# Kernel optimization log

Hardware: AMD Instinct MI355X
Metric: run time of the kernel (lower is better)

## Reference

```python
import jax, jax.numpy as jnp
import numpy as np

N, E, FD, H, NG, LAT = 20000, 320000, 64, 4, 64, 512


def _gat(x, W, a_src, a_dst, b, src, dst):
    # x: [N, in]; W: [H*FD, in]; a_src/a_dst: [H, FD]; b: [H*FD]
    h = (x @ W.T).reshape(N, H, FD)
    s = jnp.sum(h * a_src, -1)   # [N, H]
    d = jnp.sum(h * a_dst, -1)   # [N, H]
    e = jax.nn.leaky_relu(s[src] + d[dst], negative_slope=0.2)  # [E', H]
    m = jax.ops.segment_max(e, dst, num_segments=N)
    ex = jnp.exp(e - m[dst])
    den = jax.ops.segment_sum(ex, dst, num_segments=N)
    alpha = ex / den[dst]                                        # [E', H]
    out = jax.ops.segment_sum(alpha[:, :, None] * h[src], dst, num_segments=N)
    return out.reshape(N, H * FD) + b


def setup_inputs() -> dict:
    key = jax.random.key(0)
    ks = jax.random.split(key, 24)
    inp = {}
    inp['street_feature'] = jax.random.normal(ks[0], (N, 128), jnp.float32)
    inp['building_feature'] = jax.random.normal(ks[1], (N, 5), jnp.float32)
    sm = jax.random.randint(ks[2], (N, 1), 0, 2).astype(jnp.float32)
    inp['street_mask'] = sm
    inp['building_mask'] = 1.0 - sm
    inp['edge_index'] = jax.random.randint(ks[3], (2, E), 0, N, dtype=jnp.int32)
    # batch: sorted graph ids covering all NG graphs (no empty segments)
    rest = jax.random.randint(ks[4], (N - NG,), 0, NG, dtype=jnp.int32)
    inp['batch'] = jnp.sort(jnp.concatenate([jnp.arange(NG, dtype=jnp.int32), rest]))

    def lin(k, o, i):
        s = 1.0 / np.sqrt(i)
        return jax.random.uniform(k, (o, i), jnp.float32, -s, s)

    inp['street_W'] = lin(ks[5], FD, 128); inp['street_b'] = jnp.zeros((FD,), jnp.float32)
    inp['building_W'] = lin(ks[6], FD, 5); inp['building_b'] = jnp.zeros((FD,), jnp.float32)
    inp['W1'] = lin(ks[7], H * FD, FD)
    inp['a_src1'] = jax.random.normal(ks[8], (H, FD), jnp.float32) * 0.1
    inp['a_dst1'] = jax.random.normal(ks[9], (H, FD), jnp.float32) * 0.1
    inp['b1'] = jnp.zeros((H * FD,), jnp.float32)
    inp['W2'] = lin(ks[10], H * FD, H * FD)
    inp['a_src2'] = jax.random.normal(ks[11], (H, FD), jnp.float32) * 0.1
    inp['a_dst2'] = jax.random.normal(ks[12], (H, FD), jnp.float32) * 0.1
    inp['b2'] = jnp.zeros((H * FD,), jnp.float32)
    inp['W3'] = lin(ks[13], H * FD, H * FD)
    inp['a_src3'] = jax.random.normal(ks[14], (H, FD), jnp.float32) * 0.1
    inp['a_dst3'] = jax.random.normal(ks[15], (H, FD), jnp.float32) * 0.1
    inp['b3'] = jnp.zeros((H * FD,), jnp.float32)
    agg_in = FD * (1 + H * 3)  # 832
    inp['agg_W'] = lin(ks[16], LAT, agg_in); inp['agg_b'] = jnp.zeros((LAT,), jnp.float32)
    inp['mu_W'] = lin(ks[17], LAT, LAT); inp['mu_b'] = jnp.zeros((LAT,), jnp.float32)
    inp['var_W'] = lin(ks[18], LAT, LAT); inp['var_b'] = jnp.zeros((LAT,), jnp.float32)
    return inp


def reference(street_feature, building_feature, street_mask, building_mask,
              edge_index, batch,
              street_W, street_b, building_W, building_b,
              W1, a_src1, a_dst1, b1, W2, a_src2, a_dst2, b2,
              W3, a_src3, a_dst3, b3, agg_W, agg_b, mu_W, mu_b, var_W, var_b):
    sf = jax.nn.relu(street_feature @ street_W.T + street_b)
    bf = jax.nn.relu(building_feature @ building_W.T + building_b)
    n0 = sf * street_mask + bf * building_mask  # [N, FD]
    # add self loops (PyG GATConv default)
    loop = jnp.arange(N, dtype=edge_index.dtype)
    src = jnp.concatenate([edge_index[0], loop])
    dst = jnp.concatenate([edge_index[1], loop])
    n1 = jax.nn.relu(_gat(n0, W1, a_src1, a_dst1, b1, src, dst))
    n2 = jax.nn.relu(_gat(n1, W2, a_src2, a_dst2, b2, src, dst))
    n3 = jax.nn.relu(_gat(n2, W3, a_src3, a_dst3, b3, src, dst))
    g0 = jax.ops.segment_max(n0, batch, num_segments=NG)
    g1 = jax.ops.segment_max(n1, batch, num_segments=NG)
    g2 = jax.ops.segment_max(n2, batch, num_segments=NG)
    g3 = jax.ops.segment_max(n3, batch, num_segments=NG)
    g = jnp.concatenate([g0, g1, g2, g3], axis=1)  # [NG, FD*(1+3H)]
    latent = g @ agg_W.T + agg_b
    mu = latent @ mu_W.T + mu_b
    log_var = latent @ var_W.T + var_b
    return (mu, log_var)
```

## Files before the change

### kernel.cpp

```cpp
#include <hip/hip_runtime.h>
#include <math.h>

#define NNODES 20000
#define NEDGES 320000
#define FDIM 64
#define NHEAD 4
#define NGR 64
#define LATD 512
#define HF 256
#define NEP (NEDGES + NNODES)
#define AGGIN 832
#define MPAD 20032

typedef float f32x4 __attribute__((ext_vector_type(4)));
typedef short bf16x8 __attribute__((ext_vector_type(8)));
typedef unsigned short u16x8 __attribute__((ext_vector_type(8)));

__device__ inline unsigned short f2bf(float f) {
    unsigned u = __float_as_uint(f);
    unsigned r = (u + 0x7FFF + ((u >> 16) & 1)) >> 16;
    return (unsigned short)r;
}
__device__ inline float bf2f(unsigned short h) {
    return __uint_as_float(((unsigned)h) << 16);
}
__device__ inline unsigned short f2h(float f) {
    _Float16 h = (_Float16)f;
    unsigned short u;
    __builtin_memcpy(&u, &h, 2);
    return u;
}
__device__ inline float h2f(unsigned short u) {
    _Float16 h;
    __builtin_memcpy(&h, &u, 2);
    return (float)h;
}

#define EDGE_BLOCKS4 ((NEP + 1023) / 1024)
#define CONV_N (HF * FDIM + 2 * HF * HF)
#define CONV_BLOCKS ((CONV_N + 255) / 256)
#define ENC_BLOCKS (NNODES / 32)
#define GEMM_BLOCKS (NNODES / 32)
#define SLAB_BLOCKS (NNODES / 32)

__global__ void prep_kernel(
    const int* __restrict__ ei, int* __restrict__ cnt,
    const float* __restrict__ W1, const float* __restrict__ W2, const float* __restrict__ W3,
    unsigned short* __restrict__ W1hi, unsigned short* __restrict__ W1lo,
    unsigned short* __restrict__ W2hi, unsigned short* __restrict__ W2lo,
    unsigned short* __restrict__ W3hi, unsigned short* __restrict__ W3lo)
{
    if (blockIdx.x < EDGE_BLOCKS4) {
        int i0 = blockIdx.x * 1024 + threadIdx.x;
#pragma unroll
        for (int u = 0; u < 4; u++) {
            int i = i0 + u * 256;
            if (i < NEDGES) {
                atomicAdd(&cnt[ei[NEDGES + i]], 1);
            } else if (i < NEP) {
                atomicAdd(&cnt[i - NEDGES], 1);
            }
        }
    } else {
        int i = (blockIdx.x - EDGE_BLOCKS4) * 256 + threadIdx.x;
        const int n1 = HF * FDIM, n2 = HF * HF;
        const float* src; unsigned short *hi, *lo; int j;
        if (i < n1) { src = W1; hi = W1hi; lo = W1lo; j = i; }
        else if (i < n1 + n2) { src = W2; hi = W2hi; lo = W2lo; j = i - n1; }
        else if (i < n1 + 2 * n2) { src = W3; hi = W3hi; lo = W3lo; j = i - n1 - n2; }
        else return;
        float f = src[j];
        unsigned short h = f2bf(f);
        hi[j] = h;
        lo[j] = f2bf(f - bf2f(h));
    }
}

__global__ __launch_bounds__(1024) void scan_deg(const int* __restrict__ deg, int* __restrict__ offs)
{
    __shared__ int wt[16];
    const int per = (NNODES + 1023) / 1024;
    int t = threadIdx.x, lane = t & 63, w = t >> 6;
    int start = t * per;
    int end = start + per; if (end > NNODES) end = NNODES;
    int s = 0;
    for (int i = start; i < end; i++) s += deg[i];
    int pref = s;
#pragma unroll
    for (int m = 1; m < 64; m <<= 1) {
        int v = __shfl_up(pref, m, 64);
        if (lane >= m) pref += v;
    }
    if (lane == 63) wt[w] = pref;
    __syncthreads();
    int wadd = 0;
    for (int i = 0; i < w; i++) wadd += wt[i];
    int acc = wadd + pref - s;
    for (int i = start; i < end; i++) { offs[i] = acc; acc += deg[i]; }
    if (t == 1023) offs[NNODES] = NEP;
}

__global__ void scatter_edges(const int* __restrict__ ei, const int* __restrict__ offs,
                              int* __restrict__ cnt2, int* __restrict__ csr_src)
{
    int i0 = blockIdx.x * 1024 + threadIdx.x;
    int sv[4], dv[4];
#pragma unroll
    for (int u = 0; u < 4; u++) {
        int i = i0 + u * 256;
        if (i < NEDGES) { sv[u] = ei[i]; dv[u] = ei[NEDGES + i]; }
        else if (i < NEP) { sv[u] = i - NEDGES; dv[u] = i - NEDGES; }
        else { sv[u] = -1; dv[u] = 0; }
    }
#pragma unroll
    for (int u = 0; u < 4; u++) {
        if (sv[u] >= 0) {
            int p = offs[dv[u]] + atomicAdd(&cnt2[dv[u]], 1);
            csr_src[p] = sv[u];
        }
    }
}

__global__ __launch_bounds__(256) void encode_n0(
    const float* __restrict__ sfeat, const float* __restrict__ bfeat,
    const float* __restrict__ smask, const float* __restrict__ bmask,
    const float* __restrict__ sW, const float* __restrict__ sb,
    const float* __restrict__ bW, const float* __restrict__ bb,
    const int* __restrict__ batch,
    unsigned short* __restrict__ nhi, unsigned short* __restrict__ nlo,
    int* __restrict__ g)
{
    __shared__ float wlds[64 * 132];
    int t = threadIdx.x;
#pragma unroll
    for (int it = 0; it < 8; it++) {
        int idx = it * 256 + t;
        int f = idx >> 5, k4 = idx & 31;
        float4 v = *(const float4*)(sW + f * 128 + k4 * 4);
        *(float4*)(&wlds[f * 132 + k4 * 4]) = v;
    }
    __syncthreads();

    int lane = t & 63, wave = t >> 6;
    int nb = blockIdx.x * 32 + wave * 8;

    float acc[8];
#pragma unroll
    for (int i = 0; i < 8; i++) acc[i] = 0.f;

    const float* xbase = sfeat + (size_t)nb * 128;
    for (int k4 = 0; k4 < 32; k4++) {
        float4 wv = *(const float4*)(&wlds[lane * 132 + k4 * 4]);
#pragma unroll
        for (int i = 0; i < 8; i++) {
            float4 xv = *(const float4*)(xbase + i * 128 + k4 * 4);
            acc[i] += xv.x * wv.x + xv.y * wv.y + xv.z * wv.z + xv.w * wv.w;
        }
    }

    float bwr[5];
#pragma unroll
    for (int k = 0; k < 5; k++) bwr[k] = bW[lane * 5 + k];
    float sbv = sb[lane], bbv = bb[lane];

    int curb = batch[nb];
    float m = 0.f;
#pragma unroll
    for (int i = 0; i < 8; i++) {
        int node = nb + i;
        float accb = 0.f;
#pragma unroll
        for (int k = 0; k < 5; k++) accb += bfeat[node * 5 + k] * bwr[k];
        float sv = fmaxf(acc[i] + sbv, 0.f);
        float bv = fmaxf(accb + bbv, 0.f);
        float val = sv * smask[node] + bv * bmask[node];
        unsigned short hb = f2bf(val);
        nhi[(size_t)node * FDIM + lane] = hb;
        nlo[(size_t)node * FDIM + lane] = f2bf(val - bf2f(hb));
        int b = batch[node];
        if (b != curb) {
            atomicMax(&g[curb * AGGIN + lane], __float_as_int(m));
            m = 0.f; curb = b;
        }
        m = fmaxf(m, val);
    }
    atomicMax(&g[curb * AGGIN + lane], __float_as_int(m));
}

template <int K>
__global__ __launch_bounds__(256, 3) void gemm_attn_mfma(
    const unsigned short* __restrict__ xhi, const unsigned short* __restrict__ xlo,
    const unsigned short* __restrict__ Whi, const unsigned short* __restrict__ Wlo,
    const float* __restrict__ a_src, const float* __restrict__ a_dst,
    unsigned short* __restrict__ h, float* __restrict__ s, float* __restrict__ d)
{
    constexpr int NCHUNK = K / 32;
    int t = threadIdx.x, lane = t & 63, w = t >> 6;
    int colid = lane & 15, quad = lane >> 4;
    int nb = blockIdx.x * 32;

    f32x4 acc[2][4];
#pragma unroll
    for (int mt = 0; mt < 2; mt++)
#pragma unroll
        for (int nt = 0; nt < 4; nt++)
#pragma unroll
            for (int r = 0; r < 4; r++) acc[mt][nt][r] = 0.f;

    bf16x8 bhi[2][4], blo[2][4], ahi[2][2], alo[2][2];

    auto load_chunk = [&](int kc, int buf) {
#pragma unroll
        for (int nt = 0; nt < 4; nt++) {
            size_t boff = (size_t)(w * 64 + nt * 16 + colid) * K + kc + quad * 8;
            bhi[buf][nt] = *(const bf16x8*)&Whi[boff];
            blo[buf][nt] = *(const bf16x8*)&Wlo[boff];
        }
#pragma unroll
        for (int mt = 0; mt < 2; mt++) {
            size_t aoff = (size_t)(nb + mt * 16 + colid) * K + kc + quad * 8;
            ahi[buf][mt] = *(const bf16x8*)&xhi[aoff];
            alo[buf][mt] = *(const bf16x8*)&xlo[aoff];
        }
    };

    load_chunk(0, 0);
#pragma unroll
    for (int c = 0; c < NCHUNK; c++) {
        int buf = c & 1;
        if (c + 1 < NCHUNK) load_chunk((c + 1) * 32, buf ^ 1);
#pragma unroll
        for (int mt = 0; mt < 2; mt++)
#pragma unroll
            for (int nt = 0; nt < 4; nt++) {
                acc[mt][nt] = __builtin_amdgcn_mfma_f32_16x16x32_bf16(ahi[buf][mt], bhi[buf][nt], acc[mt][nt], 0, 0, 0);
                acc[mt][nt] = __builtin_amdgcn_mfma_f32_16x16x32_bf16(ahi[buf][mt], blo[buf][nt], acc[mt][nt], 0, 0, 0);
                acc[mt][nt] = __builtin_amdgcn_mfma_f32_16x16x32_bf16(alo[buf][mt], bhi[buf][nt], acc[mt][nt], 0, 0, 0);
            }
    }

#pragma unroll
    for (int mt = 0; mt < 2; mt++) {
#pragma unroll
        for (int r = 0; r < 4; r++) {
            int node = nb + mt * 16 + quad * 4 + r;
#pragma unroll
            for (int nt = 0; nt < 4; nt++)
                h[(size_t)node * HF + w * 64 + nt * 16 + colid] = f2h(acc[mt][nt][r]);
        }
    }

    float as_r[4], ad_r[4];
#pragma unroll
    for (int nt = 0; nt < 4; nt++) {
        as_r[nt] = a_src[w * 64 + nt * 16 + colid];
        ad_r[nt] = a_dst[w * 64 + nt * 16 + colid];
    }
#pragma unroll
    for (int mt = 0; mt < 2; mt++) {
#pragma unroll
        for (int r = 0; r < 4; r++) {
            float ps = 0.f, pd = 0.f;
#pragma unroll
            for (int nt = 0; nt < 4; nt++) {
                ps += acc[mt][nt][r] * as_r[nt];
                pd += acc[mt][nt][r] * ad_r[nt];
            }
#pragma unroll
            for (int m = 1; m < 16; m <<= 1) {
                ps += __shfl_xor(ps, m, 64);
                pd += __shfl_xor(pd, m, 64);
            }
            if (colid == 0) {
                int node = nb + mt * 16 + quad * 4 + r;
                s[(size_t)node * NHEAD + w] = ps;
                d[(size_t)node * NHEAD + w] = pd;
            }
        }
    }
}

__global__ __launch_bounds__(256) void gat_aggr(
    const unsigned short* __restrict__ h, const float* __restrict__ s, const float* __restrict__ d,
    const int* __restrict__ offs, const int* __restrict__ csr_src,
    const float* __restrict__ bias,
    unsigned short* __restrict__ ohi, unsigned short* __restrict__ olo)
{
    int t = threadIdx.x;
    int lane = t & 63;
    int wv = t >> 6;
    int node = blockIdx.x * 4 + wv;
    int eh = lane >> 5;
    int p = lane & 31;
    int hd2 = p >> 3;
    int f0 = p * 8;
    int lo = offs[node], hi = offs[node + 1];
    int deg = hi - lo;

    float a[8];
#pragma unroll
    for (int j = 0; j < 8; j++) a[j] = 0.f;
    float inv;

    if (deg <= 64) {
        int slot = lane >> 2, hd = lane & 3;
        float dn = d[(size_t)node * NHEAD + hd];
        float ev[4];
        int sv[4];
#pragma unroll
        for (int c = 0; c < 4; c++) {
            int k = c * 16 + slot;
            float e = -3.402823466e38f;
            int src = 0;
            if (k < deg) {
                src = csr_src[lo + k];
                float ee = s[(size_t)src * NHEAD + hd] + dn;
                e = fmaxf(ee, 0.2f * ee);
            }
            ev[c] = e; sv[c] = src;
        }
        float mx = fmaxf(fmaxf(ev[0], ev[1]), fmaxf(ev[2], ev[3]));
#pragma unroll
        for (int m = 4; m < 64; m <<= 1) mx = fmaxf(mx, __shfl_xor(mx, m, 64));
        float den = 0.f;
#pragma unroll
        for (int c = 0; c < 4; c++) {
            ev[c] = __expf(ev[c] - mx);
            den += ev[c];
        }
#pragma unroll
        for (int m = 4; m < 64; m <<= 1) den += __shfl_xor(den, m, 64);

        inv = 1.f / __shfl(den, hd2);

#pragma unroll
        for (int c = 0; c < 4; c++) {
            int base = c * 16;
            if (base >= deg) break;
            int n16 = deg - base; if (n16 > 16) n16 = 16;
            for (int kk = 0; kk < n16; kk += 8) {
                float ex[4]; int sr[4]; u16x8 hv[4];
#pragma unroll
                for (int u = 0; u < 4; u++) {
                    int sl = (kk + u * 2 + eh) * 4 + hd2;
                    ex[u] = __shfl(ev[c], sl);
                    sr[u] = __shfl(sv[c], sl);
                }
#pragma unroll
                for (int u = 0; u < 4; u++)
                    hv[u] = *(const u16x8*)(h + (size_t)sr[u] * HF + f0);
#pragma unroll
                for (int u = 0; u < 4; u++)
#pragma unroll
                    for (int j = 0; j < 8; j++) a[j] += ex[u] * h2f(hv[u][j]);
            }
        }
    } else {
        float dn2 = d[(size_t)node * NHEAD + hd2];
        float mx = -3.402823466e38f;
        for (int i = lo; i < hi; i++) {
            int src = csr_src[i];
            float e = s[(size_t)src * NHEAD + hd2] + dn2;
            e = fmaxf(e, 0.2f * e);
            mx = fmaxf(mx, e);
        }
        float den = 0.f;
        for (int i = lo + eh; i < hi; i += 2) {
            int src = csr_src[i];
            float e = s[(size_t)src * NHEAD + hd2] + dn2;
            e = fmaxf(e, 0.2f * e);
            float ex = __expf(e - mx);
            den += ex;
            u16x8 hv = *(const u16x8*)(h + (size_t)src * HF + f0);
#pragma unroll
            for (int j = 0; j < 8; j++) a[j] += ex * h2f(hv[j]);
        }
        den += __shfl_xor(den, 32, 64);
        inv = 1.f / den;
    }

#pragma unroll
    for (int j = 0; j < 8; j++) a[j] += __shfl_xor(a[j], 32, 64);

    if (eh == 0) {
        float v[8];
#pragma unroll
        for (int j = 0; j < 8; j++) v[j] = fmaxf(a[j] * inv + bias[f0 + j], 0.f);
        ushort4 hb0, lb0, hb1, lb1;
        hb0.x = f2bf(v[0]); lb0.x = f2bf(v[0] - bf2f(hb0.x));
        hb0.y = f2bf(v[1]); lb0.y = f2bf(v[1] - bf2f(hb0.y));
        hb0.z = f2bf(v[2]); lb0.z = f2bf(v[2] - bf2f(hb0.z));
        hb0.w = f2bf(v[3]); lb0.w = f2bf(v[3] - bf2f(hb0.w));
        hb1.x = f2bf(v[4]); lb1.x = f2bf(v[4] - bf2f(hb1.x));
        hb1.y = f2bf(v[5]); lb1.y = f2bf(v[5] - bf2f(hb1.y));
        hb1.z = f2bf(v[6]); lb1.z = f2bf(v[6] - bf2f(hb1.z));
        hb1.w = f2bf(v[7]); lb1.w = f2bf(v[7] - bf2f(hb1.w));
        *(ushort4*)(ohi + (size_t)node * HF + f0) = hb0;
        *(ushort4*)(ohi + (size_t)node * HF + f0 + 4) = hb1;
        *(ushort4*)(olo + (size_t)node * HF + f0) = lb0;
        *(ushort4*)(olo + (size_t)node * HF + f0 + 4) = lb1;
    }
}

__global__ __launch_bounds__(256) void seg_max_slab_bf(
    const unsigned short* __restrict__ xhi, const unsigned short* __restrict__ xlo,
    const int* __restrict__ batch, int* __restrict__ g, int coloff)
{
    int f = threadIdx.x;
    int r0 = blockIdx.x * 32;
    int cur = batch[r0];
    float m = 0.f;
    for (int r = r0; r < r0 + 32; r += 4) {
        float v[4]; int bb[4];
#pragma unroll
        for (int i = 0; i < 4; i++) {
            size_t idx = (size_t)(r + i) * HF + f;
            v[i] = bf2f(xhi[idx]) + bf2f(xlo[idx]);
            bb[i] = batch[r + i];
        }
#pragma unroll
        for (int i = 0; i < 4; i++) {
            if (bb[i] != cur) {
                atomicMax(&g[cur * AGGIN + coloff + f], __float_as_int(m));
                m = 0.f; cur = bb[i];
            }
            m = fmaxf(m, v[i]);
        }
    }
    atomicMax(&g[cur * AGGIN + coloff + f], __float_as_int(m));
}

__global__ __launch_bounds__(256) void mlp_latent(
    const float* __restrict__ g, const float* __restrict__ W, const float* __restrict__ b,
    float* __restrict__ latent)
{
    int idx = blockIdx.x * 256 + threadIdx.x;
    int r = idx >> 9, c = idx & 511;
    const float4* gv = (const float4*)(g + (size_t)r * AGGIN);
    const float4* wv = (const float4*)(W + (size_t)c * AGGIN);
    float acc = 0.f;
#pragma unroll 4
    for (int k = 0; k < AGGIN / 4; k++) {
        float4 a = gv[k], w = wv[k];
        acc += a.x * w.x + a.y * w.y + a.z * w.z + a.w * w.w;
    }
    latent[idx] = acc + b[c];
}

__global__ __launch_bounds__(256) void mlp_head(
    const float* __restrict__ latent,
    const float* __restrict__ muW, const float* __restrict__ mub,
    const float* __restrict__ vW, const float* __restrict__ vb,
    float* __restrict__ out)
{
    int idx = blockIdx.x * 256 + threadIdx.x;
    int half = idx >> 15;
    int j = idx & 32767;
    int r = j >> 9, c = j & 511;
    const float* W = half ? vW : muW;
    const float* bb = half ? vb : mub;
    const float4* lv = (const float4*)(latent + (size_t)r * LATD);
    const float4* wv = (const float4*)(W + (size_t)c * LATD);
    float acc = 0.f;
#pragma unroll 4
    for (int k = 0; k < LATD / 4; k++) {
        float4 a = lv[k], w = wv[k];
        acc += a.x * w.x + a.y * w.y + a.z * w.z + a.w * w.w;
    }
    out[idx] = acc + bb[c];
}

static inline size_t align16(size_t x) { return (x + 15) & ~(size_t)15; }

extern "C" void kernel_launch(void* const* d_in, const int* in_sizes, int n_in,
                              void* d_out, int out_size, void* d_ws, size_t ws_size,
                              hipStream_t stream)
{
    const float* sfeat = (const float*)d_in[0];
    const float* bfeat = (const float*)d_in[1];
    const float* smask = (const float*)d_in[2];
    const float* bmask = (const float*)d_in[3];
    const int*   ei    = (const int*)d_in[4];
    const int*   batch = (const int*)d_in[5];
    const float* sW = (const float*)d_in[6];
    const float* sb = (const float*)d_in[7];
    const float* bW = (const float*)d_in[8];
    const float* bb = (const float*)d_in[9];
    const float* W1 = (const float*)d_in[10];
    const float* as1 = (const float*)d_in[11];
    const float* ad1 = (const float*)d_in[12];
    const float* b1 = (const float*)d_in[13];
    const float* W2 = (const float*)d_in[14];
    const float* as2 = (const float*)d_in[15];
    const float* ad2 = (const float*)d_in[16];
    const float* b2 = (const float*)d_in[17];
    const float* W3 = (const float*)d_in[18];
    const float* as3 = (const float*)d_in[19];
    const float* ad3 = (const float*)d_in[20];
    const float* b3 = (const float*)d_in[21];
    const float* aggW = (const float*)d_in[22];
    const float* aggb = (const float*)d_in[23];
    const float* muW = (const float*)d_in[24];
    const float* mub = (const float*)d_in[25];
    const float* vW = (const float*)d_in[26];
    const float* vb = (const float*)d_in[27];
    float* out = (float*)d_out;

    char* ws = (char*)d_ws;
    size_t off = 0;
    unsigned short* h = (unsigned short*)(ws + off); off = align16(off + (size_t)NNODES * HF * 2);
    unsigned short* Ahi = (unsigned short*)(ws + off); off = align16(off + (size_t)MPAD * HF * 2);
    unsigned short* Alo = (unsigned short*)(ws + off); off = align16(off + (size_t)MPAD * HF * 2);
    float* s  = (float*)(ws + off); off = align16(off + (size_t)NNODES * NHEAD * 4);
    float* d  = (float*)(ws + off); off = align16(off + (size_t)NNODES * NHEAD * 4);
    int* offs = (int*)(ws + off);   off = align16(off + (size_t)(NNODES + 1) * 4);
    size_t zstart = off;
    int* cnt  = (int*)(ws + off);   off = align16(off + (size_t)NNODES * 4);
    int* cnt2 = (int*)(ws + off);   off = align16(off + (size_t)NNODES * 4);
    float* g  = (float*)(ws + off); off = align16(off + (size_t)NGR * AGGIN * 4);
    size_t zbytes = off - zstart;
    int* csr  = (int*)(ws + off);   off = align16(off + (size_t)NEP * 4);
    float* lat = (float*)(ws + off); off = align16(off + (size_t)NGR * LATD * 4);
    unsigned short* W1hi = (unsigned short*)(ws + off); off = align16(off + (size_t)HF * FDIM * 2);
    unsigned short* W1lo = (unsigned short*)(ws + off); off = align16(off + (size_t)HF * FDIM * 2);
    unsigned short* W2hi = (unsigned short*)(ws + off); off = align16(off + (size_t)HF * HF * 2);
    unsigned short* W2lo = (unsigned short*)(ws + off); off = align16(off + (size_t)HF * HF * 2);
    unsigned short* W3hi = (unsigned short*)(ws + off); off = align16(off + (size_t)HF * HF * 2);
    unsigned short* W3lo = (unsigned short*)(ws + off); off = align16(off + (size_t)HF * HF * 2);

    hipMemsetAsync(ws + zstart, 0, zbytes, stream);

    prep_kernel<<<EDGE_BLOCKS4 + CONV_BLOCKS, 256, 0, stream>>>(
        ei, cnt, W1, W2, W3, W1hi, W1lo, W2hi, W2lo, W3hi, W3lo);
    scan_deg<<<1, 1024, 0, stream>>>(cnt, offs);
    scatter_edges<<<EDGE_BLOCKS4, 256, 0, stream>>>(ei, offs, cnt2, csr);
    encode_n0<<<ENC_BLOCKS, 256, 0, stream>>>(
        sfeat, bfeat, smask, bmask, sW, sb, bW, bb, batch, Ahi, Alo, (int*)g);

    gemm_attn_mfma<FDIM><<<GEMM_BLOCKS, 256, 0, stream>>>(
        Ahi, Alo, W1hi, W1lo, as1, ad1, h, s, d);
    gat_aggr<<<NNODES / 4, 256, 0, stream>>>(h, s, d, offs, csr, b1, Ahi, Alo);
    seg_max_slab_bf<<<SLAB_BLOCKS, 256, 0, stream>>>(Ahi, Alo, batch, (int*)g, FDIM);

    gemm_attn_mfma<HF><<<GEMM_BLOCKS, 256, 0, stream>>>(
        Ahi, Alo, W2hi, W2lo, as2, ad2, h, s, d);
    gat_aggr<<<NNODES / 4, 256, 0, stream>>>(h, s, d, offs, csr, b2, Ahi, Alo);
    seg_max_slab_bf<<<SLAB_BLOCKS, 256, 0, stream>>>(Ahi, Alo, batch, (int*)g, FDIM + HF);

    gemm_attn_mfma<HF><<<GEMM_BLOCKS, 256, 0, stream>>>(
        Ahi, Alo, W3hi, W3lo, as3, ad3, h, s, d);
    gat_aggr<<<NNODES / 4, 256, 0, stream>>>(h, s, d, offs, csr, b3, Ahi, Alo);
    seg_max_slab_bf<<<SLAB_BLOCKS, 256, 0, stream>>>(Ahi, Alo, batch, (int*)g, FDIM + 2 * HF);

    mlp_latent<<<(NGR * LATD + 255) / 256, 256, 0, stream>>>(g, aggW, aggb, lat);
    mlp_head<<<(2 * NGR * LATD + 255) / 256, 256, 0, stream>>>(lat, muW, mub, vW, vb, out);
}
```

Measured before the change: 431.2 us.

## Batch full 64-wide K chunk loads before MFMAs in GAT projection GEMM

Replaces the double-buffered 32-wide K-chunk prefetch with a scheme that issues all global loads for a 64-wide K chunk up front, then runs all the MFMAs for that chunk behind a sched_barrier. It also lowers the launch-bounds occupancy hint from 3 to 2 blocks per CU so the larger register footprint fits. The aim is more memory-level parallelism per wave and fewer load/compute interleaving stalls. In exchange, loads and MFMAs across chunks no longer overlap within a wave, and fewer waves are resident to hide latency.

```diff
diff --git a/kernel.cpp b/kernel.cpp
--- a/kernel.cpp
+++ b/kernel.cpp
@@ -188,13 +188,13 @@
 }
 
 template <int K>
-__global__ __launch_bounds__(256, 3) void gemm_attn_mfma(
+__global__ __launch_bounds__(256, 2) void gemm_attn_mfma(
     const unsigned short* __restrict__ xhi, const unsigned short* __restrict__ xlo,
     const unsigned short* __restrict__ Whi, const unsigned short* __restrict__ Wlo,
     const float* __restrict__ a_src, const float* __restrict__ a_dst,
     unsigned short* __restrict__ h, float* __restrict__ s, float* __restrict__ d)
 {
-    constexpr int NCHUNK = K / 32;
+    constexpr int NCHUNK = K / 64;
     int t = threadIdx.x, lane = t & 63, w = t >> 6;
     int colid = lane & 15, quad = lane >> 4;
     int nb = blockIdx.x * 32;
@@ -207,36 +207,36 @@
 #pragma unroll
             for (int r = 0; r < 4; r++) acc[mt][nt][r] = 0.f;
 
-    bf16x8 bhi[2][4], blo[2][4], ahi[2][2], alo[2][2];
-
-    auto load_chunk = [&](int kc, int buf) {
-#pragma unroll
-        for (int nt = 0; nt < 4; nt++) {
-            size_t boff = (size_t)(w * 64 + nt * 16 + colid) * K + kc + quad * 8;
-            bhi[buf][nt] = *(const bf16x8*)&Whi[boff];
-            blo[buf][nt] = *(const bf16x8*)&Wlo[boff];
-        }
-#pragma unroll
-        for (int mt = 0; mt < 2; mt++) {
-            size_t aoff = (size_t)(nb + mt * 16 + colid) * K + kc + quad * 8;
-            ahi[buf][mt] = *(const bf16x8*)&xhi[aoff];
-            alo[buf][mt] = *(const bf16x8*)&xlo[aoff];
-        }
-    };
-
-    load_chunk(0, 0);
 #pragma unroll
     for (int c = 0; c < NCHUNK; c++) {
-        int buf = c & 1;
-        if (c + 1 < NCHUNK) load_chunk((c + 1) * 32, buf ^ 1);
-#pragma unroll
-        for (int mt = 0; mt < 2; mt++)
+        const int kc = c * 64;
+        bf16x8 bh[4][2], bl[4][2], ah[2][2], al[2][2];
+#pragma unroll
+        for (int half = 0; half < 2; half++) {
+#pragma unroll
+            for (int mt = 0; mt < 2; mt++) {
+                size_t aoff = (size_t)(nb + mt * 16 + colid) * K + kc + half * 32 + quad * 8;
+                ah[mt][half] = *(const bf16x8*)&xhi[aoff];
+                al[mt][half] = *(const bf16x8*)&xlo[aoff];
+            }
 #pragma unroll
             for (int nt = 0; nt < 4; nt++) {
-                acc[mt][nt] = __builtin_amdgcn_mfma_f32_16x16x32_bf16(ahi[buf][mt], bhi[buf][nt], acc[mt][nt], 0, 0, 0);
-                acc[mt][nt] = __builtin_amdgcn_mfma_f32_16x16x32_bf16(ahi[buf][mt], blo[buf][nt], acc[mt][nt], 0, 0, 0);
-                acc[mt][nt] = __builtin_amdgcn_mfma_f32_16x16x32_bf16(alo[buf][mt], bhi[buf][nt], acc[mt][nt], 0, 0, 0);
-            }
+                size_t boff = (size_t)(w * 64 + nt * 16 + colid) * K + kc + half * 32 + quad * 8;
+                bh[nt][half] = *(const bf16x8*)&Whi[boff];
+                bl[nt][half] = *(const bf16x8*)&Wlo[boff];
+            }
+        }
+        __builtin_amdgcn_sched_barrier(0);
+#pragma unroll
+        for (int half = 0; half < 2; half++)
+#pragma unroll
+            for (int mt = 0; mt < 2; mt++)
+#pragma unroll
+                for (int nt = 0; nt < 4; nt++) {
+                    acc[mt][nt] = __builtin_amdgcn_mfma_f32_16x16x32_bf16(ah[mt][half], bh[nt][half], acc[mt][nt], 0, 0, 0);
+                    acc[mt][nt] = __builtin_amdgcn_mfma_f32_16x16x32_bf16(ah[mt][half], bl[nt][half], acc[mt][nt], 0, 0, 0);
+                    acc[mt][nt] = __builtin_amdgcn_mfma_f32_16x16x32_bf16(al[mt][half], bh[nt][half], acc[mt][nt], 0, 0, 0);
+                }
     }
 
 #pragma unroll
```

Measured after the change: 432.3 us. About the same (+0.2%).
